# Performance work log

Hardware: AMD Instinct MI355X
Metric: run time of the kernel (lower is better)

## Reference

```python
import jax, jax.numpy as jnp
import numpy as np

S = 2048  # expert group size
M = 768   # hidden size
H = 3072  # intermediate size
E = 16    # num experts


def top2_gating(gates):
    # gates: [G, S, E]
    G, S_, E_ = gates.shape
    C = 2 * S_ // E_
    mask_dtype = jnp.int32
    index_1 = jnp.argmax(gates, axis=-1)
    mask_1 = jax.nn.one_hot(index_1, E_, dtype=mask_dtype)
    gate_1 = jnp.einsum('GSE,GSE->GS', gates, mask_1)
    gates_without_top_1 = gates * (1 - mask_1)
    index_2 = jnp.argmax(gates_without_top_1, axis=-1)
    mask_2 = jax.nn.one_hot(index_2, E_, dtype=mask_dtype)
    gate_2 = jnp.einsum('GSE,GSE->GS', gates_without_top_1, mask_2)
    pos_1 = jnp.cumsum(mask_1, axis=-2) - mask_1
    mask_1 = mask_1 * (pos_1 < C)
    pos_1 = jnp.einsum('GSE,GSE->GS', pos_1, mask_1)
    mask_1_count = jnp.sum(mask_1, axis=-2)
    mask_1_flat = jnp.sum(mask_1, axis=-1)
    pos_2 = jnp.cumsum(mask_2, axis=-2) - mask_2 + jnp.expand_dims(mask_1_count, -2)
    mask_2 = mask_2 * (pos_2 < C)
    pos_2 = jnp.einsum('GSE,GSE->GS', pos_2, mask_2)
    mask_2_flat = jnp.sum(mask_2, axis=-1)
    gate_1 = gate_1 * mask_1_flat
    gate_2 = gate_2 * mask_2_flat
    denom = gate_1 + gate_2
    denom = jnp.where(denom > 0, denom, jnp.ones_like(denom))
    gate_1 = gate_1 / denom
    gate_2 = gate_2 / denom
    a = jnp.expand_dims(gate_1 * mask_1_flat, -1) * jax.nn.one_hot(index_1, E_, dtype=gates.dtype)
    b = jax.nn.one_hot(pos_1, C, dtype=gates.dtype)
    first = jnp.einsum('GSE,GSC->GSEC', a, b)
    a = jnp.expand_dims(gate_2 * mask_2_flat, -1) * jax.nn.one_hot(index_2, E_, dtype=gates.dtype)
    b = jax.nn.one_hot(pos_2, C, dtype=gates.dtype)
    second = jnp.einsum('GSE,GSC->GSEC', a, b)
    combined_tensor = first + second
    dispatch_tensor = combined_tensor.astype(jnp.bool_)
    return combined_tensor, dispatch_tensor


def setup_inputs() -> dict:
    key = jax.random.key(0)
    k1, k2, k3, k4 = jax.random.split(key, 4)
    inputs = jax.random.normal(k1, (4, 1024, M), dtype=jnp.float32)
    wg = jax.random.normal(k2, (M, E), dtype=jnp.float32) * (1.0 / np.sqrt(M))
    wi = jax.random.normal(k3, (E, M, H), dtype=jnp.float32) * (1.0 / np.sqrt(M))
    wo = jax.random.normal(k4, (E, H, M), dtype=jnp.float32) * (1.0 / np.sqrt(H))
    return {"inputs": inputs, "wg": wg, "wi": wi, "wo": wo}


def reference(inputs, wg, wi, wo):
    x = jnp.reshape(inputs, (-1, S, M))                      # [G, S, M]
    gates = jax.nn.softmax(jnp.einsum('GSM,ME->GSE', x, wg))
    combined_weights, dispatch_mask = top2_gating(gates)
    dispatched = jnp.einsum('GSEC,GSM->EGCM',
                            dispatch_mask.astype(x.dtype), x)
    h = jnp.einsum('EGCM,EMH->EGCH', dispatched, wi)
    h = jax.nn.relu(h)
    expert_out = jnp.einsum('EGCH,EHM->GECM', h, wo)
    out = jnp.einsum('GSEC,GECM->GSM', combined_weights, expert_out)
    return jnp.reshape(out, inputs.shape)
```

## Files before the change

kernel.cpp:

```cpp
#include <hip/hip_runtime.h>
#include <hip/hip_bf16.h>
#include <cstdint>
#include <cstddef>

#define S_TOK 2048
#define M_DIM 768
#define H_DIM 3072
#define E_NUM 16
#define CAP   256

using s16x8 = __attribute__((ext_vector_type(8))) short;
using f32x4 = __attribute__((ext_vector_type(4))) float;

__device__ __forceinline__ unsigned short f2bf(float f) {
    unsigned u = __float_as_uint(f);
    unsigned r = 0x7fffu + ((u >> 16) & 1u);
    return (unsigned short)((u + r) >> 16);
}

__device__ __forceinline__ void async16(const void* g, void* l) {
    __builtin_amdgcn_global_load_lds((const __attribute__((address_space(1))) void*)g,
                                     (__attribute__((address_space(3))) void*)l, 16, 0, 0);
}

__global__ void gating_kernel(const float* __restrict__ x, const float* __restrict__ wg,
                              int* __restrict__ e1o, int* __restrict__ e2o,
                              float* __restrict__ g1o, float* __restrict__ g2o,
                              unsigned short* __restrict__ xb, int ntok) {
    if (blockIdx.x == 0) {
        for (int m = threadIdx.x; m < M_DIM; m += blockDim.x)
            xb[(size_t)ntok * M_DIM + m] = 0;
    }
    int gid  = blockIdx.x * blockDim.x + threadIdx.x;
    int tok  = gid >> 6;
    int lane = threadIdx.x & 63;
    if (tok >= ntok) return;
    const float* xr = x + (size_t)tok * M_DIM;
    unsigned short* xbr = xb + (size_t)tok * M_DIM;
    float acc[E_NUM];
#pragma unroll
    for (int e = 0; e < E_NUM; ++e) acc[e] = 0.f;
    for (int m = lane; m < M_DIM; m += 64) {
        float xv = xr[m];
        xbr[m] = f2bf(xv);
        const float* wr = wg + (size_t)m * E_NUM;
#pragma unroll
        for (int e = 0; e < E_NUM; ++e) acc[e] += xv * wr[e];
    }
#pragma unroll
    for (int off = 32; off >= 1; off >>= 1) {
#pragma unroll
        for (int e = 0; e < E_NUM; ++e) acc[e] += __shfl_xor(acc[e], off, 64);
    }
    if (lane == 0) {
        float mx = acc[0];
#pragma unroll
        for (int e = 1; e < E_NUM; ++e) mx = fmaxf(mx, acc[e]);
        float p[E_NUM]; float s = 0.f;
#pragma unroll
        for (int e = 0; e < E_NUM; ++e) { p[e] = expf(acc[e] - mx); s += p[e]; }
        float inv = 1.f / s;
        int b1 = 0; float v1 = -1.f;
#pragma unroll
        for (int e = 0; e < E_NUM; ++e) { if (p[e] > v1) { v1 = p[e]; b1 = e; } }
        int b2 = 0; float v2 = -1.f;
#pragma unroll
        for (int e = 0; e < E_NUM; ++e) { if (e != b1 && p[e] > v2) { v2 = p[e]; b2 = e; } }
        e1o[tok] = b1; e2o[tok] = b2;
        g1o[tok] = v1 * inv; g2o[tok] = v2 * inv;
    }
}

__global__ void assign_kernel(const int* __restrict__ e1a, const int* __restrict__ e2a,
                              const float* __restrict__ g1a, const float* __restrict__ g2a,
                              int* __restrict__ slot1, int* __restrict__ slot2,
                              float* __restrict__ wslot,
                              int* __restrict__ tfs, int G) {
    int g    = blockIdx.x;
    int tid  = threadIdx.x;
    int w    = tid >> 6;
    int lane = tid & 63;
    __shared__ int cnt1s[E_NUM];

    for (int i = tid; i < E_NUM * CAP; i += 1024) tfs[(size_t)g * E_NUM * CAP + i] = -1;
    __syncthreads();

    {
        int vals[S_TOK / 64];
#pragma unroll
        for (int it = 0; it < S_TOK / 64; ++it) vals[it] = e1a[g * S_TOK + it * 64 + lane];
        int cnt = 0;
#pragma unroll
        for (int it = 0; it < S_TOK / 64; ++it) {
            int base = it * 64;
            int t = g * S_TOK + base + lane;
            bool pred = (vals[it] == w);
            unsigned long long bal = __ballot(pred);
            int prefix = __popcll(bal & ((1ull << lane) - 1ull));
            if (pred) {
                int pos = cnt + prefix;
                if (pos < CAP) {
                    slot1[t] = w * CAP + pos;
                    tfs[((size_t)g * E_NUM + w) * CAP + pos] = base + lane;
                } else {
                    slot1[t] = -1;
                }
            }
            cnt += __popcll(bal);
        }
        if (lane == 0) cnt1s[w] = cnt < CAP ? cnt : CAP;
    }
    __syncthreads();
    {
        int vals[S_TOK / 64];
#pragma unroll
        for (int it = 0; it < S_TOK / 64; ++it) vals[it] = e2a[g * S_TOK + it * 64 + lane];
        int cnt = cnt1s[w];
#pragma unroll
        for (int it = 0; it < S_TOK / 64; ++it) {
            int base = it * 64;
            int t = g * S_TOK + base + lane;
            bool pred = (vals[it] == w);
            unsigned long long bal = __ballot(pred);
            int prefix = __popcll(bal & ((1ull << lane) - 1ull));
            if (pred) {
                int pos = cnt + prefix;
                if (pos < CAP) {
                    slot2[t] = w * CAP + pos;
                    tfs[((size_t)g * E_NUM + w) * CAP + pos] = base + lane;
                } else {
                    slot2[t] = -1;
                }
            }
            cnt += __popcll(bal);
        }
    }
    __syncthreads();
    for (int t = tid; t < S_TOK; t += 1024) {
        int gt = g * S_TOK + t;
        int s1 = slot1[gt], s2 = slot2[gt];
        float a = s1 >= 0 ? g1a[gt] : 0.f;
        float b = s2 >= 0 ? g2a[gt] : 0.f;
        float denom = a + b;
        if (!(denom > 0.f)) denom = 1.f;
        if (s1 >= 0) wslot[(size_t)g * E_NUM * CAP + s1] = a / denom;
        if (s2 >= 0) wslot[(size_t)g * E_NUM * CAP + s2] = b / denom;
    }
}

__global__ __launch_bounds__(256) void transpose_conv_kernel(const float* __restrict__ src,
                                                             unsigned short* __restrict__ dst,
                                                             int R, int C) {
    __shared__ float T[64][65];
    int e  = blockIdx.z;
    int c0 = blockIdx.x * 64;
    int r0 = blockIdx.y * 64;
    int tid = threadIdx.x;
    int lx = tid & 63, ly = tid >> 6;
    const float* S = src + (size_t)e * R * C;
#pragma unroll
    for (int i = 0; i < 16; ++i) {
        int r = i * 4 + ly;
        T[r][lx] = S[(size_t)(r0 + r) * C + c0 + lx];
    }
    __syncthreads();
    unsigned short* D = dst + (size_t)e * C * R;
#pragma unroll
    for (int i = 0; i < 16; ++i) {
        int c = i * 4 + ly;
        D[(size_t)(c0 + c) * R + r0 + lx] = f2bf(T[lx][c]);
    }
}

__global__ __launch_bounds__(512) void gemm1_kernel(
        const unsigned short* __restrict__ A,
        const unsigned short* __restrict__ B,
        const int* __restrict__ tfs,
        unsigned short* __restrict__ Hout, int G) {
    __shared__ unsigned short As[256 * 32];
    __shared__ unsigned short Bs[128 * 32];
    __shared__ int rowtok[256];

    int e  = blockIdx.z;
    int n0 = (blockIdx.x >> 1) * 128;
    int g  = blockIdx.x & 1;
    int z  = e * G + g;
    int tid = threadIdx.x;

    if (tid < 256) rowtok[tid] = tfs[((size_t)g * E_NUM + e) * CAP + tid];
    __syncthreads();

    int r4 = tid >> 2, l4 = tid & 3;
    int t0 = rowtok[r4], t1 = rowtok[128 + r4];
    size_t row0 = (t0 < 0) ? (size_t)(G * S_TOK) : (size_t)(g * S_TOK + t0);
    size_t row1 = (t1 < 0) ? (size_t)(G * S_TOK) : (size_t)(g * S_TOK + t1);
    const unsigned short* apt0 = A + row0 * M_DIM + l4 * 8;
    const unsigned short* apt1 = A + row1 * M_DIM + l4 * 8;
    const unsigned short* bpt  = B + (size_t)e * H_DIM * M_DIM + ((size_t)n0 + r4) * M_DIM + l4 * 8;

    int wv = tid >> 6;
    unsigned short* as0 = &As[(wv * 16) * 32];
    unsigned short* as1 = &As[(128 + wv * 16) * 32];
    unsigned short* bs  = &Bs[(wv * 16) * 32];

    int lane = tid & 63;
    int r = lane & 15, q = lane >> 4;
    int wm = wv & 3, wn = wv >> 2;

    f32x4 acc[4][4];
#pragma unroll
    for (int i = 0; i < 4; ++i)
#pragma unroll
        for (int j = 0; j < 4; ++j) acc[i][j] = (f32x4)(0.f);

    for (int k0 = 0; k0 < M_DIM; k0 += 32) {
        async16(apt0, as0);
        async16(apt1, as1);
        async16(bpt, bs);
        apt0 += 32; apt1 += 32; bpt += 32;
        __syncthreads();
        s16x8 af[4], bfr[4];
#pragma unroll
        for (int i = 0; i < 4; ++i)
            af[i] = *(const s16x8*)&As[(wm * 64 + i * 16 + r) * 32 + q * 8];
#pragma unroll
        for (int j = 0; j < 4; ++j)
            bfr[j] = *(const s16x8*)&Bs[(wn * 64 + j * 16 + r) * 32 + q * 8];
#pragma unroll
        for (int i = 0; i < 4; ++i)
#pragma unroll
            for (int j = 0; j < 4; ++j)
                acc[i][j] = __builtin_amdgcn_mfma_f32_16x16x32_bf16(af[i], bfr[j], acc[i][j], 0, 0, 0);
        __syncthreads();
    }

#pragma unroll
    for (int i = 0; i < 4; ++i) {
#pragma unroll
        for (int v = 0; v < 4; ++v) {
            int m_loc = wm * 64 + i * 16 + q * 4 + v;
            unsigned short* row = Hout + ((size_t)z * CAP + m_loc) * H_DIM + n0;
#pragma unroll
            for (int j = 0; j < 4; ++j) {
                int n_loc = wn * 64 + j * 16 + r;
                row[n_loc] = f2bf(fmaxf(acc[i][j][v], 0.f));
            }
        }
    }
}

__global__ void zero_kernel(float4* __restrict__ p, int n4) {
    int i = blockIdx.x * blockDim.x + threadIdx.x;
    if (i < n4) p[i] = make_float4(0.f, 0.f, 0.f, 0.f);
}

__global__ __launch_bounds__(256) void gemm2_kernel(
        const unsigned short* __restrict__ A,
        const unsigned short* __restrict__ B,
        const int* __restrict__ tfs,
        const float* __restrict__ wslot,
        float* __restrict__ out, int G) {
    __shared__ unsigned short As[128 * 32];
    __shared__ unsigned short Bs[128 * 32];
    __shared__ int   rowtok[128];
    __shared__ float rowwt[128];

    int e  = blockIdx.z & 15;
    int kc = blockIdx.z >> 4;
    int n0 = blockIdx.x * 128;
    int c0 = (blockIdx.y >> 1) * 128;
    int g  = blockIdx.y & 1;
    int z  = e * G + g;
    int tid = threadIdx.x;

    if (tid < 128) {
        size_t sidx = ((size_t)g * E_NUM + e) * CAP + c0 + tid;
        rowtok[tid] = tfs[sidx];
        rowwt[tid]  = wslot[sidx];
    }

    const int KC = H_DIM / 2;
    int kb = kc * KC;
    int r4 = tid >> 2, l4 = tid & 3;
    const unsigned short* apt0 = A + ((size_t)z * CAP + c0 + r4) * H_DIM + kb + l4 * 8;
    const unsigned short* apt1 = apt0 + (size_t)64 * H_DIM;
    const unsigned short* bpt0 = B + (size_t)e * M_DIM * H_DIM + ((size_t)n0 + r4) * H_DIM + kb + l4 * 8;
    const unsigned short* bpt1 = bpt0 + (size_t)64 * H_DIM;

    int wv = tid >> 6;
    unsigned short* as0 = &As[(wv * 16) * 32];
    unsigned short* as1 = &As[(64 + wv * 16) * 32];
    unsigned short* bs0 = &Bs[(wv * 16) * 32];
    unsigned short* bs1 = &Bs[(64 + wv * 16) * 32];

    int lane = tid & 63;
    int r = lane & 15, q = lane >> 4;
    int wm = wv & 1, wn = wv >> 1;

    f32x4 acc[4][4];
#pragma unroll
    for (int i = 0; i < 4; ++i)
#pragma unroll
        for (int j = 0; j < 4; ++j) acc[i][j] = (f32x4)(0.f);

    for (int k0 = 0; k0 < KC; k0 += 32) {
        async16(apt0, as0);
        async16(apt1, as1);
        async16(bpt0, bs0);
        async16(bpt1, bs1);
        apt0 += 32; apt1 += 32; bpt0 += 32; bpt1 += 32;
        __syncthreads();
        s16x8 af[4], bfr[4];
#pragma unroll
        for (int i = 0; i < 4; ++i)
            af[i] = *(const s16x8*)&As[(wm * 64 + i * 16 + r) * 32 + q * 8];
#pragma unroll
        for (int j = 0; j < 4; ++j)
            bfr[j] = *(const s16x8*)&Bs[(wn * 64 + j * 16 + r) * 32 + q * 8];
#pragma unroll
        for (int i = 0; i < 4; ++i)
#pragma unroll
            for (int j = 0; j < 4; ++j)
                acc[i][j] = __builtin_amdgcn_mfma_f32_16x16x32_bf16(af[i], bfr[j], acc[i][j], 0, 0, 0);
        __syncthreads();
    }

#pragma unroll
    for (int i = 0; i < 4; ++i) {
#pragma unroll
        for (int v = 0; v < 4; ++v) {
            int m_loc = wm * 64 + i * 16 + q * 4 + v;
            int tok = rowtok[m_loc];
            if (tok < 0) continue;
            float w = rowwt[m_loc];
            float* orow = out + ((size_t)(g * S_TOK + tok)) * M_DIM + n0;
#pragma unroll
            for (int j = 0; j < 4; ++j) {
                int n_loc = wn * 64 + j * 16 + r;
                atomicAdd(&orow[n_loc], w * acc[i][j][v]);
            }
        }
    }
}

extern "C" void kernel_launch(void* const* d_in, const int* in_sizes, int n_in,
                              void* d_out, int out_size, void* d_ws, size_t ws_size,
                              hipStream_t stream) {
    const float* x  = (const float*)d_in[0];
    const float* wg = (const float*)d_in[1];
    const float* wi = (const float*)d_in[2];
    const float* wo = (const float*)d_in[3];
    float* out = (float*)d_out;

    int ntok = in_sizes[0] / M_DIM;
    int G = ntok / S_TOK;

    char* wsp = (char*)d_ws;
    auto carve = [&](size_t bytes) {
        void* p = (void*)wsp;
        wsp += (bytes + 255) & ~(size_t)255;
        return p;
    };
    int*   e1    = (int*)carve((size_t)ntok * 4);
    int*   e2    = (int*)carve((size_t)ntok * 4);
    float* g1    = (float*)carve((size_t)ntok * 4);
    float* g2    = (float*)carve((size_t)ntok * 4);
    int*   slot1 = (int*)carve((size_t)ntok * 4);
    int*   slot2 = (int*)carve((size_t)ntok * 4);
    float* wslot = (float*)carve((size_t)G * E_NUM * CAP * 4);
    int*   tfs   = (int*)carve((size_t)G * E_NUM * CAP * 4);
    unsigned short* xb  = (unsigned short*)carve((size_t)(ntok + 1) * M_DIM * 2);
    unsigned short* wiT = (unsigned short*)carve((size_t)E_NUM * H_DIM * M_DIM * 2);
    unsigned short* woT = (unsigned short*)carve((size_t)E_NUM * M_DIM * H_DIM * 2);
    unsigned short* h   = (unsigned short*)carve((size_t)E_NUM * G * CAP * H_DIM * 2);

    gating_kernel<<<(ntok * 64 + 255) / 256, 256, 0, stream>>>(x, wg, e1, e2, g1, g2, xb, ntok);
    assign_kernel<<<G, 1024, 0, stream>>>(e1, e2, g1, g2, slot1, slot2, wslot, tfs, G);

    transpose_conv_kernel<<<dim3(H_DIM / 64, M_DIM / 64, E_NUM), 256, 0, stream>>>(wi, wiT, M_DIM, H_DIM);
    transpose_conv_kernel<<<dim3(M_DIM / 64, H_DIM / 64, E_NUM), 256, 0, stream>>>(wo, woT, H_DIM, M_DIM);

    gemm1_kernel<<<dim3((H_DIM / 128) * 2, 1, E_NUM), 512, 0, stream>>>(xb, wiT, tfs, h, G);

    int n4 = ntok * M_DIM / 4;
    zero_kernel<<<(n4 + 255) / 256, 256, 0, stream>>>((float4*)out, n4);

    gemm2_kernel<<<dim3(M_DIM / 128, 2 * 2, 2 * E_NUM), 256, 0, stream>>>(h, woT, tfs, wslot, out, G);
}
```

Measured before the change: 567.8 us.

## Retile expert GEMMs with XCD-aware block mapping and K=64 steps

Both expert GEMMs move to 128x128 tiles with 256 threads. Blocks are mapped so that the four (capacity-half, group) tiles sharing one weight slice land on the same XCD, which should improve L2 reuse of the bf16 weights. Each K iteration now loads 64 elements into two LDS buffers, halving the number of barriers, and gemm2 splits K four ways to raise parallelism at the cost of more atomic adds. The weight transpose store is also widened to write two bf16 values per thread.

```diff
diff --git a/kernel.cpp b/kernel.cpp
--- a/kernel.cpp
+++ b/kernel.cpp
@@ -165,72 +165,94 @@
     }
     __syncthreads();
     unsigned short* D = dst + (size_t)e * C * R;
-#pragma unroll
-    for (int i = 0; i < 16; ++i) {
-        int c = i * 4 + ly;
-        D[(size_t)(c0 + c) * R + r0 + lx] = f2bf(T[lx][c]);
-    }
-}
-
-__global__ __launch_bounds__(512) void gemm1_kernel(
+    int r2 = (tid & 31) * 2;
+    int cy = tid >> 5;
+#pragma unroll
+    for (int i = 0; i < 8; ++i) {
+        int c = i * 8 + cy;
+        ushort2 v;
+        v.x = f2bf(T[r2][c]);
+        v.y = f2bf(T[r2 + 1][c]);
+        *(ushort2*)&D[(size_t)(c0 + c) * R + r0 + r2] = v;
+    }
+}
+
+
+__global__ __launch_bounds__(256) void gemm1_kernel(
         const unsigned short* __restrict__ A,
         const unsigned short* __restrict__ B,
         const int* __restrict__ tfs,
-        unsigned short* __restrict__ Hout, int G) {
-    __shared__ unsigned short As[256 * 32];
-    __shared__ unsigned short Bs[128 * 32];
-    __shared__ int rowtok[256];
-
-    int e  = blockIdx.z;
-    int n0 = (blockIdx.x >> 1) * 128;
-    int g  = blockIdx.x & 1;
-    int z  = e * G + g;
-    int tid = threadIdx.x;
-
-    if (tid < 256) rowtok[tid] = tfs[((size_t)g * E_NUM + e) * CAP + tid];
+        unsigned short* __restrict__ Hout, int G, int ntok) {
+    __shared__ unsigned short As0[128 * 32], As1[128 * 32];
+    __shared__ unsigned short Bs0[128 * 32], Bs1[128 * 32];
+    __shared__ int rowtok[128];
+
+    int bx   = blockIdx.x;
+    int xcd  = bx & 7;
+    int slot = bx >> 3;
+    int t    = (slot >> 2) * 8 + xcd;
+    int j    = slot & 3;
+    int e    = t / 24;
+    int n0   = (t % 24) * 128;
+    int c0   = (j >> 1) * 128;
+    int g    = j & 1;
+    int z    = e * G + g;
+    int tid  = threadIdx.x;
+
+    if (tid < 128) rowtok[tid] = tfs[((size_t)g * E_NUM + e) * CAP + c0 + tid];
     __syncthreads();
 
-    int r4 = tid >> 2, l4 = tid & 3;
-    int t0 = rowtok[r4], t1 = rowtok[128 + r4];
-    size_t row0 = (t0 < 0) ? (size_t)(G * S_TOK) : (size_t)(g * S_TOK + t0);
-    size_t row1 = (t1 < 0) ? (size_t)(G * S_TOK) : (size_t)(g * S_TOK + t1);
-    const unsigned short* apt0 = A + row0 * M_DIM + l4 * 8;
-    const unsigned short* apt1 = A + row1 * M_DIM + l4 * 8;
-    const unsigned short* bpt  = B + (size_t)e * H_DIM * M_DIM + ((size_t)n0 + r4) * M_DIM + l4 * 8;
-
-    int wv = tid >> 6;
-    unsigned short* as0 = &As[(wv * 16) * 32];
-    unsigned short* as1 = &As[(128 + wv * 16) * 32];
-    unsigned short* bs  = &Bs[(wv * 16) * 32];
+    int w = tid >> 6, l = tid & 63;
+    int rA  = 16 * w + (l >> 2);
+    int seg = l & 3;
+
+    const unsigned short* aRow[2];
+    const unsigned short* bRow[2];
+#pragma unroll
+    for (int p = 0; p < 2; ++p) {
+        int tok = rowtok[p * 64 + rA];
+        size_t grow = (tok < 0) ? (size_t)ntok : (size_t)(g * S_TOK + tok);
+        aRow[p] = A + grow * M_DIM + seg * 8;
+        bRow[p] = B + (size_t)e * H_DIM * M_DIM + ((size_t)n0 + p * 64 + rA) * M_DIM + seg * 8;
+    }
+    unsigned aoff = w * 512 + 0;
 
     int lane = tid & 63;
     int r = lane & 15, q = lane >> 4;
-    int wm = wv & 3, wn = wv >> 2;
+    int wm = w & 1, wn = w >> 1;
 
     f32x4 acc[4][4];
 #pragma unroll
     for (int i = 0; i < 4; ++i)
 #pragma unroll
-        for (int j = 0; j < 4; ++j) acc[i][j] = (f32x4)(0.f);
-
-    for (int k0 = 0; k0 < M_DIM; k0 += 32) {
-        async16(apt0, as0);
-        async16(apt1, as1);
-        async16(bpt, bs);
-        apt0 += 32; apt1 += 32; bpt += 32;
+        for (int jj = 0; jj < 4; ++jj) acc[i][jj] = (f32x4)(0.f);
+
+    for (int k0 = 0; k0 < M_DIM; k0 += 64) {
+#pragma unroll
+        for (int p = 0; p < 2; ++p) {
+            async16(aRow[p] + k0,      As0 + p * 2048 + aoff);
+            async16(aRow[p] + k0 + 32, As1 + p * 2048 + aoff);
+            async16(bRow[p] + k0,      Bs0 + p * 2048 + aoff);
+            async16(bRow[p] + k0 + 32, Bs1 + p * 2048 + aoff);
+        }
         __syncthreads();
-        s16x8 af[4], bfr[4];
-#pragma unroll
-        for (int i = 0; i < 4; ++i)
-            af[i] = *(const s16x8*)&As[(wm * 64 + i * 16 + r) * 32 + q * 8];
-#pragma unroll
-        for (int j = 0; j < 4; ++j)
-            bfr[j] = *(const s16x8*)&Bs[(wn * 64 + j * 16 + r) * 32 + q * 8];
-#pragma unroll
-        for (int i = 0; i < 4; ++i)
-#pragma unroll
-            for (int j = 0; j < 4; ++j)
-                acc[i][j] = __builtin_amdgcn_mfma_f32_16x16x32_bf16(af[i], bfr[j], acc[i][j], 0, 0, 0);
+#pragma unroll
+        for (int kk = 0; kk < 2; ++kk) {
+            const unsigned short* Asb = kk ? As1 : As0;
+            const unsigned short* Bsb = kk ? Bs1 : Bs0;
+            s16x8 af[4], bfr[4];
+#pragma unroll
+            for (int i = 0; i < 4; ++i)
+                af[i] = *(const s16x8*)&Asb[(wm * 64 + i * 16 + r) * 32 + q * 8];
+#pragma unroll
+            for (int jj = 0; jj < 4; ++jj)
+                bfr[jj] = *(const s16x8*)&Bsb[(wn * 64 + jj * 16 + r) * 32 + q * 8];
+#pragma unroll
+            for (int i = 0; i < 4; ++i)
+#pragma unroll
+                for (int jj = 0; jj < 4; ++jj)
+                    acc[i][jj] = __builtin_amdgcn_mfma_f32_16x16x32_bf16(af[i], bfr[jj], acc[i][jj], 0, 0, 0);
+        }
         __syncthreads();
     }
 
@@ -239,19 +261,14 @@
 #pragma unroll
         for (int v = 0; v < 4; ++v) {
             int m_loc = wm * 64 + i * 16 + q * 4 + v;
-            unsigned short* row = Hout + ((size_t)z * CAP + m_loc) * H_DIM + n0;
-#pragma unroll
-            for (int j = 0; j < 4; ++j) {
-                int n_loc = wn * 64 + j * 16 + r;
-                row[n_loc] = f2bf(fmaxf(acc[i][j][v], 0.f));
+            unsigned short* row = Hout + ((size_t)z * CAP + c0 + m_loc) * H_DIM + n0;
+#pragma unroll
+            for (int jj = 0; jj < 4; ++jj) {
+                int n_loc = wn * 64 + jj * 16 + r;
+                row[n_loc] = f2bf(fmaxf(acc[i][jj][v], 0.f));
             }
         }
     }
-}
-
-__global__ void zero_kernel(float4* __restrict__ p, int n4) {
-    int i = blockIdx.x * blockDim.x + threadIdx.x;
-    if (i < n4) p[i] = make_float4(0.f, 0.f, 0.f, 0.f);
 }
 
 __global__ __launch_bounds__(256) void gemm2_kernel(
@@ -260,18 +277,24 @@
         const int* __restrict__ tfs,
         const float* __restrict__ wslot,
         float* __restrict__ out, int G) {
-    __shared__ unsigned short As[128 * 32];
-    __shared__ unsigned short Bs[128 * 32];
+    __shared__ unsigned short As0[128 * 32], As1[128 * 32];
+    __shared__ unsigned short Bs0[128 * 32], Bs1[128 * 32];
     __shared__ int   rowtok[128];
     __shared__ float rowwt[128];
 
-    int e  = blockIdx.z & 15;
-    int kc = blockIdx.z >> 4;
-    int n0 = blockIdx.x * 128;
-    int c0 = (blockIdx.y >> 1) * 128;
-    int g  = blockIdx.y & 1;
-    int z  = e * G + g;
-    int tid = threadIdx.x;
+    int bx   = blockIdx.x;
+    int xcd  = bx & 7;
+    int slot = bx >> 3;
+    int t    = (slot >> 2) * 8 + xcd;
+    int j    = slot & 3;
+    int e    = t / 24;
+    int rem  = t % 24;
+    int kc   = rem / 6;
+    int n0   = (rem % 6) * 128;
+    int c0   = (j >> 1) * 128;
+    int g    = j & 1;
+    int z    = e * G + g;
+    int tid  = threadIdx.x;
 
     if (tid < 128) {
         size_t sidx = ((size_t)g * E_NUM + e) * CAP + c0 + tid;
@@ -279,49 +302,57 @@
         rowwt[tid]  = wslot[sidx];
     }
 
-    const int KC = H_DIM / 2;
+    int w = tid >> 6, l = tid & 63;
+    int rA  = 16 * w + (l >> 2);
+    int seg = l & 3;
+    const int KC = H_DIM / 4;
     int kb = kc * KC;
-    int r4 = tid >> 2, l4 = tid & 3;
-    const unsigned short* apt0 = A + ((size_t)z * CAP + c0 + r4) * H_DIM + kb + l4 * 8;
-    const unsigned short* apt1 = apt0 + (size_t)64 * H_DIM;
-    const unsigned short* bpt0 = B + (size_t)e * M_DIM * H_DIM + ((size_t)n0 + r4) * H_DIM + kb + l4 * 8;
-    const unsigned short* bpt1 = bpt0 + (size_t)64 * H_DIM;
-
-    int wv = tid >> 6;
-    unsigned short* as0 = &As[(wv * 16) * 32];
-    unsigned short* as1 = &As[(64 + wv * 16) * 32];
-    unsigned short* bs0 = &Bs[(wv * 16) * 32];
-    unsigned short* bs1 = &Bs[(64 + wv * 16) * 32];
+
+    const unsigned short* aRow[2];
+    const unsigned short* bRow[2];
+#pragma unroll
+    for (int p = 0; p < 2; ++p) {
+        aRow[p] = A + ((size_t)z * CAP + c0 + p * 64 + rA) * H_DIM + kb + seg * 8;
+        bRow[p] = B + (size_t)e * M_DIM * H_DIM + ((size_t)n0 + p * 64 + rA) * H_DIM + kb + seg * 8;
+    }
+    unsigned aoff = w * 512;
 
     int lane = tid & 63;
     int r = lane & 15, q = lane >> 4;
-    int wm = wv & 1, wn = wv >> 1;
+    int wm = w & 1, wn = w >> 1;
 
     f32x4 acc[4][4];
 #pragma unroll
     for (int i = 0; i < 4; ++i)
 #pragma unroll
-        for (int j = 0; j < 4; ++j) acc[i][j] = (f32x4)(0.f);
-
-    for (int k0 = 0; k0 < KC; k0 += 32) {
-        async16(apt0, as0);
-        async16(apt1, as1);
-        async16(bpt0, bs0);
-        async16(bpt1, bs1);
-        apt0 += 32; apt1 += 32; bpt0 += 32; bpt1 += 32;
+        for (int jj = 0; jj < 4; ++jj) acc[i][jj] = (f32x4)(0.f);
+
+    for (int k0 = 0; k0 < KC; k0 += 64) {
+#pragma unroll
+        for (int p = 0; p < 2; ++p) {
+            async16(aRow[p] + k0,      As0 + p * 2048 + aoff);
+            async16(aRow[p] + k0 + 32, As1 + p * 2048 + aoff);
+            async16(bRow[p] + k0,      Bs0 + p * 2048 + aoff);
+            async16(bRow[p] + k0 + 32, Bs1 + p * 2048 + aoff);
+        }
         __syncthreads();
-        s16x8 af[4], bfr[4];
-#pragma unroll
-        for (int i = 0; i < 4; ++i)
-            af[i] = *(const s16x8*)&As[(wm * 64 + i * 16 + r) * 32 + q * 8];
-#pragma unroll
-        for (int j = 0; j < 4; ++j)
-            bfr[j] = *(const s16x8*)&Bs[(wn * 64 + j * 16 + r) * 32 + q * 8];
-#pragma unroll
-        for (int i = 0; i < 4; ++i)
-#pragma unroll
-            for (int j = 0; j < 4; ++j)
-                acc[i][j] = __builtin_amdgcn_mfma_f32_16x16x32_bf16(af[i], bfr[j], acc[i][j], 0, 0, 0);
+#pragma unroll
+        for (int kk = 0; kk < 2; ++kk) {
+            const unsigned short* Asb = kk ? As1 : As0;
+            const unsigned short* Bsb = kk ? Bs1 : Bs0;
+            s16x8 af[4], bfr[4];
+#pragma unroll
+            for (int i = 0; i < 4; ++i)
+                af[i] = *(const s16x8*)&Asb[(wm * 64 + i * 16 + r) * 32 + q * 8];
+#pragma unroll
+            for (int jj = 0; jj < 4; ++jj)
+                bfr[jj] = *(const s16x8*)&Bsb[(wn * 64 + jj * 16 + r) * 32 + q * 8];
+#pragma unroll
+            for (int i = 0; i < 4; ++i)
+#pragma unroll
+                for (int jj = 0; jj < 4; ++jj)
+                    acc[i][jj] = __builtin_amdgcn_mfma_f32_16x16x32_bf16(af[i], bfr[jj], acc[i][jj], 0, 0, 0);
+        }
         __syncthreads();
     }
 
@@ -332,15 +363,20 @@
             int m_loc = wm * 64 + i * 16 + q * 4 + v;
             int tok = rowtok[m_loc];
             if (tok < 0) continue;
-            float w = rowwt[m_loc];
+            float wgt = rowwt[m_loc];
             float* orow = out + ((size_t)(g * S_TOK + tok)) * M_DIM + n0;
 #pragma unroll
-            for (int j = 0; j < 4; ++j) {
-                int n_loc = wn * 64 + j * 16 + r;
-                atomicAdd(&orow[n_loc], w * acc[i][j][v]);
+            for (int jj = 0; jj < 4; ++jj) {
+                int n_loc = wn * 64 + jj * 16 + r;
+                atomicAdd(&orow[n_loc], wgt * acc[i][jj][v]);
             }
         }
     }
+}
+
+__global__ void zero_kernel(float4* __restrict__ p, int n4) {
+    int i = blockIdx.x * blockDim.x + threadIdx.x;
+    if (i < n4) p[i] = make_float4(0.f, 0.f, 0.f, 0.f);
 }
 
 extern "C" void kernel_launch(void* const* d_in, const int* in_sizes, int n_in,
@@ -380,10 +416,10 @@
     transpose_conv_kernel<<<dim3(H_DIM / 64, M_DIM / 64, E_NUM), 256, 0, stream>>>(wi, wiT, M_DIM, H_DIM);
     transpose_conv_kernel<<<dim3(M_DIM / 64, H_DIM / 64, E_NUM), 256, 0, stream>>>(wo, woT, H_DIM, M_DIM);
 
-    gemm1_kernel<<<dim3((H_DIM / 128) * 2, 1, E_NUM), 512, 0, stream>>>(xb, wiT, tfs, h, G);
+    gemm1_kernel<<<1536, 256, 0, stream>>>(xb, wiT, tfs, h, G, ntok);
 
     int n4 = ntok * M_DIM / 4;
     zero_kernel<<<(n4 + 255) / 256, 256, 0, stream>>>((float4*)out, n4);
 
-    gemm2_kernel<<<dim3(M_DIM / 128, 2 * 2, 2 * E_NUM), 256, 0, stream>>>(h, woT, tfs, wslot, out, G);
-}
+    gemm2_kernel<<<1536, 256, 0, stream>>>(h, woT, tfs, wslot, out, G);
+}
```

New measurement: 553.0 us. 2.6% less time.
